# Optimization experiments

Measured on AMD Instinct MI355X. Metric: run time of the kernel, lower is better.

## Reference

```python
import jax, jax.numpy as jnp
import numpy as np

RCUT = 6.0
NMAX = 8
LMAX = 6
SIGMA = 0.5
BOX = 30.0
N_ATOMS = 3072


def setup_inputs() -> dict:
    key = jax.random.key(0)
    k1, k2 = jax.random.split(key)
    positions = jax.random.uniform(k1, (N_ATOMS, 3), dtype=jnp.float32) * BOX
    atom_types = jax.random.randint(k2, (N_ATOMS,), 0, 8, dtype=jnp.int64)
    cell = BOX * jnp.eye(3, dtype=jnp.float32)
    return {"positions": positions, "atom_types": atom_types, "cell": cell}


def reference(positions, atom_types, cell):
    # positions: [N,3], cell: [3,3]; atom_types unused in the math (as in original).
    n = positions.shape[0]
    diff = positions[:, None, :] - positions[None, :, :]          # [N,N,3]
    # periodic minimum-image convention
    inv_cell = jnp.linalg.inv(cell)
    frac = diff @ inv_cell
    frac = frac - jnp.round(frac)
    diff = frac @ cell
    d = jnp.sqrt(jnp.sum(diff * diff, axis=-1) + 1e-10)           # [N,N]
    mask = (d < RCUT) & (d > 0.1)                                  # neighbor mask
    alpha = 0.5 / (SIGMA ** 2)
    ns = jnp.arange(NMAX, dtype=d.dtype)                           # [nmax]
    # GTO radial basis: (d/rcut)^n * exp(-alpha d^2), masked to neighbors
    gto = (d / RCUT)[None] ** ns[:, None, None] * jnp.exp(-alpha * d * d)[None]  # [nmax,N,N]
    gto = jnp.where(mask[None], gto, jnp.zeros((), dtype=d.dtype))
    # per-atom layout: concat over n of per-neighbor features -> [N, nmax*N]
    radial = jnp.transpose(gto, (1, 0, 2)).reshape(n, NMAX * n)
    angular = jnp.zeros((n, LMAX + 1), dtype=d.dtype)
    return jnp.concatenate([radial, angular], axis=1)              # [N, nmax*N + lmax+1]
```

## Files before the change

### kernel.cpp

```cpp
#include <hip/hip_runtime.h>
#include <hip/hip_bf16.h>
#include <math.h>


#define N_ATOMS 3072
#define NMAX    8
#define LP1     7
#define ROWLEN  (NMAX * N_ATOMS + LP1)
#define RCUT_F  6.0f
#define ALPHA_F 2.0f

__global__ __launch_bounds__(256)
void soap_kernel(const float* __restrict__ pos,
                 const float* __restrict__ cell,
                 float* __restrict__ out) {
    const int i = blockIdx.x;
    const int j = blockIdx.y * blockDim.x + threadIdx.x;

    const float c0 = cell[0], c1 = cell[4], c2 = cell[8];

    const float pix = pos[3 * i + 0];
    const float piy = pos[3 * i + 1];
    const float piz = pos[3 * i + 2];
    const float pjx = pos[3 * j + 0];
    const float pjy = pos[3 * j + 1];
    const float pjz = pos[3 * j + 2];

    float dx = pix - pjx;
    float dy = piy - pjy;
    float dz = piz - pjz;
    dx -= c0 * rintf(dx / c0);
    dy -= c1 * rintf(dy / c1);
    dz -= c2 * rintf(dz / c2);

    const float d2 = dx * dx + dy * dy + dz * dz + 1e-10f;
    const float d  = sqrtf(d2);
    const bool  m  = (d < RCUT_F) && (d > 0.1f);

    const float base = m ? expf(-ALPHA_F * d2) : 0.0f;
    const float r    = d * (1.0f / RCUT_F);

    size_t off = (size_t)i * ROWLEN + (size_t)j;
    float v = base;
#pragma unroll
    for (int n = 0; n < NMAX; ++n) {
        out[off] = v;
        v *= r;
        off += N_ATOMS;
    }

    if (blockIdx.y == 0 && threadIdx.x < LP1) {
        out[(size_t)i * ROWLEN + (size_t)(NMAX * N_ATOMS) + threadIdx.x] = 0.0f;
    }
}

extern "C" void kernel_launch(void* const* d_in, const int* in_sizes, int n_in,
                              void* d_out, int out_size, void* d_ws, size_t ws_size,
                              hipStream_t stream) {
    const float* pos  = (const float*)d_in[0];
    const float* cell = (const float*)d_in[2];
    float* out = (float*)d_out;

    dim3 block(256);
    dim3 grid(N_ATOMS, N_ATOMS / 256);
    soap_kernel<<<grid, block, 0, stream>>>(pos, cell, out);
}
```

Before: 53.15 us.

## Emit aligned float4 stores with four neighbors per thread and row-phase handling

Each thread now computes four consecutive neighbors and writes each radial order as a 16-byte float4 store. Because the row length of 24583 floats shifts alignment from row to row, the starting j is offset by (i & 3) so the stores stay aligned, and leftover edge columns are written with scalar stores by a few spare threads. The grid shrinks to three blocks per row, and the kernel also switches to fast __expf and reciprocal multiplies for the periodic wrap. The goal is fewer, wider store instructions on a kernel bound by output writes, at the cost of more complex indexing and a slightly less accurate exponential.

```diff
diff --git a/kernel.cpp b/kernel.cpp
--- a/kernel.cpp
+++ b/kernel.cpp
@@ -10,47 +10,78 @@
 #define RCUT_F  6.0f
 #define ALPHA_F 2.0f
 
+__device__ __forceinline__ void pair_vals(float pix, float piy, float piz,
+                                          const float* __restrict__ pos, int j,
+                                          float c0, float c1, float c2,
+                                          float ic0, float ic1, float ic2,
+                                          float& v0, float& r) {
+    float dx = pix - pos[3 * j + 0];
+    float dy = piy - pos[3 * j + 1];
+    float dz = piz - pos[3 * j + 2];
+    dx -= c0 * rintf(dx * ic0);
+    dy -= c1 * rintf(dy * ic1);
+    dz -= c2 * rintf(dz * ic2);
+    const float d2 = dx * dx + dy * dy + dz * dz + 1e-10f;
+    const float d  = sqrtf(d2);
+    const bool  m  = (d < RCUT_F) && (d > 0.1f);
+    v0 = m ? __expf(-ALPHA_F * d2) : 0.0f;
+    r  = d * (1.0f / RCUT_F);
+}
+
 __global__ __launch_bounds__(256)
-void soap_kernel(const float* __restrict__ pos,
-                 const float* __restrict__ cell,
-                 float* __restrict__ out) {
+void soap_kernel_v2(const float* __restrict__ pos,
+                    const float* __restrict__ cell,
+                    float* __restrict__ out) {
     const int i = blockIdx.x;
-    const int j = blockIdx.y * blockDim.x + threadIdx.x;
+    const int g = blockIdx.y * 256 + threadIdx.x;
 
     const float c0 = cell[0], c1 = cell[4], c2 = cell[8];
+    const float ic0 = 1.0f / c0, ic1 = 1.0f / c1, ic2 = 1.0f / c2;
 
     const float pix = pos[3 * i + 0];
     const float piy = pos[3 * i + 1];
     const float piz = pos[3 * i + 2];
-    const float pjx = pos[3 * j + 0];
-    const float pjy = pos[3 * j + 1];
-    const float pjz = pos[3 * j + 2];
 
-    float dx = pix - pjx;
-    float dy = piy - pjy;
-    float dz = piz - pjz;
-    dx -= c0 * rintf(dx / c0);
-    dy -= c1 * rintf(dy / c1);
-    dz -= c2 * rintf(dz / c2);
-
-    const float d2 = dx * dx + dy * dy + dz * dz + 1e-10f;
-    const float d  = sqrtf(d2);
-    const bool  m  = (d < RCUT_F) && (d > 0.1f);
-
-    const float base = m ? expf(-ALPHA_F * d2) : 0.0f;
-    const float r    = d * (1.0f / RCUT_F);
-
-    size_t off = (size_t)i * ROWLEN + (size_t)j;
-    float v = base;
-#pragma unroll
-    for (int n = 0; n < NMAX; ++n) {
-        out[off] = v;
-        v *= r;
-        off += N_ATOMS;
-    }
+    const int p = i & 3;
+    const int G = (p == 0) ? 768 : 767;
 
     if (blockIdx.y == 0 && threadIdx.x < LP1) {
         out[(size_t)i * ROWLEN + (size_t)(NMAX * N_ATOMS) + threadIdx.x] = 0.0f;
+    }
+
+    if (g < G) {
+        const int j0 = p + 4 * g;
+        float v[4], r[4];
+#pragma unroll
+        for (int e = 0; e < 4; ++e) {
+            pair_vals(pix, piy, piz, pos, j0 + e, c0, c1, c2, ic0, ic1, ic2,
+                      v[e], r[e]);
+        }
+        size_t off = (size_t)i * ROWLEN + (size_t)j0;
+#pragma unroll
+        for (int n = 0; n < NMAX; ++n) {
+            float4 q = make_float4(v[0], v[1], v[2], v[3]);
+            *reinterpret_cast<float4*>(out + off) = q;
+            v[0] *= r[0]; v[1] *= r[1]; v[2] *= r[2]; v[3] *= r[3];
+            off += N_ATOMS;
+        }
+    } else if (p != 0) {
+        int jb[4];
+        int c = 0;
+        for (int j = 0; j < p; ++j)        jb[c++] = j;
+        for (int j = p + 3068; j < 3072; ++j) jb[c++] = j;
+        for (int e = 0; e < 4; ++e) {
+            float v, r;
+            pair_vals(pix, piy, piz, pos, jb[e], c0, c1, c2, ic0, ic1, ic2,
+                      v, r);
+            size_t off = (size_t)i * ROWLEN + (size_t)jb[e];
+#pragma unroll
+            for (int n = 0; n < NMAX; ++n) {
+                out[off] = v;
+                v *= r;
+                off += N_ATOMS;
+            }
+        }
     }
 }
 
@@ -62,6 +93,6 @@
     float* out = (float*)d_out;
 
     dim3 block(256);
-    dim3 grid(N_ATOMS, N_ATOMS / 256);
-    soap_kernel<<<grid, block, 0, stream>>>(pos, cell, out);
+    dim3 grid(N_ATOMS, 3);
+    soap_kernel_v2<<<grid, block, 0, stream>>>(pos, cell, out);
 }
```

After: 55.05 us. 3.6% more time.
